# Kernel tuning notes

Hardware: AMD Instinct MI355X
Metric: run time of the kernel (lower is better)

Reference implementation:

```python
import jax, jax.numpy as jnp
from jax import lax
import numpy as np

# dims
B, S, IN, E = 2, 2048, 512, 1024
INNER = 2 * E              # mLSTM up-projection, proj_factor = 2.0
NH = 4                     # mLSTM cell heads
DH = INNER // NH           # 512
QKV_BLK = 4                # qkv_proj_blocksize
NHW = INNER // QKV_BLK     # heads of block-diagonal (headwise) q/k/v projections
K = 4                      # causal conv1d kernel size
EPS = 1e-6                 # mLSTM cell eps
LN_EPS = 1e-5


def setup_inputs() -> dict:
    key = jax.random.key(0)
    ks = jax.random.split(key, 16)
    n = lambda k, shp, s=0.02: jax.random.normal(k, shp, jnp.float32) * s
    z = lambda shp: jnp.zeros(shp, jnp.float32)
    return dict(
        x=jax.random.normal(ks[0], (B, S, IN), jnp.float32),
        w_in=n(ks[1], (IN, E)), b_in=z((E,)),
        ln1_w=jnp.ones((E,), jnp.float32),
        w_up=n(ks[2], (E, 2 * INNER)), b_up=z((2 * INNER,)),
        conv_w=n(ks[3], (INNER, K), 0.1), conv_b=z((INNER,)),
        q_w=n(ks[4], (NHW, QKV_BLK, QKV_BLK), 0.3), q_b=z((INNER,)),
        k_w=n(ks[5], (NHW, QKV_BLK, QKV_BLK), 0.3), k_b=z((INNER,)),
        v_w=n(ks[6], (NHW, QKV_BLK, QKV_BLK), 0.3), v_b=z((INNER,)),
        ig_w=n(ks[7], (3 * INNER, NH)), ig_b=z((NH,)),
        fg_w=n(ks[8], (3 * INNER, NH)), fg_b=jnp.ones((NH,), jnp.float32),
        onorm_w=jnp.ones((INNER,), jnp.float32),
        skip=n(ks[9], (INNER,), 1.0),
        w_down=n(ks[10], (INNER, E)), b_down=z((E,)),
        post_w=jnp.ones((E,), jnp.float32),
    )


def _layernorm(x, w, eps=LN_EPS):
    m = x.mean(-1, keepdims=True)
    v = x.var(-1, keepdims=True)
    return (x - m) / jnp.sqrt(v + eps) * w


def _headwise(x, w, b):
    # block-diagonal linear: x (B,S,INNER) split into NHW blocks of QKV_BLK
    Bx, Sx, _ = x.shape
    y = jnp.einsum('bshd,hod->bsho', x.reshape(Bx, Sx, NHW, QKV_BLK), w)
    return y.reshape(Bx, Sx, INNER) + b


def _mlstm_parallel(q, k, v, ig, fg):
    # q,k,v: (B,NH,S,DH); ig,fg: (B,NH,S). Parallel (stabilized) mLSTM.
    log_f = jax.nn.log_sigmoid(fg)                       # (B,NH,S)
    cum = jnp.cumsum(log_f, axis=-1)                     # inclusive cumsum
    dmat = cum[..., :, None] - cum[..., None, :]         # F_i - F_j  (B,NH,S,S)
    mask = jnp.tril(jnp.ones((S, S), bool))
    logD = jnp.where(mask, dmat + ig[..., None, :], -jnp.inf)
    m = logD.max(-1, keepdims=True)                      # (B,NH,S,1)
    Dm = jnp.exp(logD - m)
    qk = jnp.einsum('bnid,bnjd->bnij', q, k) / jnp.sqrt(jnp.float32(DH))
    C = qk * Dm
    norm = jnp.maximum(jnp.abs(C.sum(-1, keepdims=True)), jnp.exp(-m))
    return jnp.einsum('bnij,bnjd->bnid', C / (norm + EPS), v)


def _forward(x, w_in, b_in, ln1_w, w_up, b_up, conv_w, conv_b,
             q_w, q_b, k_w, k_b, v_w, v_b, ig_w, ig_b, fg_w, fg_b,
             onorm_w, skip, w_down, b_down, post_w):
    h_in = x @ w_in + b_in                               # (B,S,E); dropout = identity (eval)

    # --- mLSTM block: residual + pre-LN ---
    xn = _layernorm(h_in, ln1_w)
    up = xn @ w_up + b_up                                # (B,S,2*INNER)
    x_m, z = jnp.split(up, 2, axis=-1)

    # causal depthwise conv1d + SiLU
    rhs = conv_w.T[:, None, :]                           # (K,1,INNER)
    xc = lax.conv_general_dilated(x_m, rhs, window_strides=(1,),
                                  padding=[(K - 1, 0)],
                                  dimension_numbers=('NHC', 'HIO', 'NHC'),
                                  feature_group_count=INNER) + conv_b
    x_conv_act = jax.nn.silu(xc)

    q = _headwise(x_conv_act, q_w, q_b)                  # (B,S,INNER)
    k = _headwise(x_conv_act, k_w, k_b)
    v = _headwise(x_m, v_w, v_b)

    if_in = jnp.concatenate([q, k, v], axis=-1)          # (B,S,3*INNER)
    ig = (if_in @ ig_w + ig_b).transpose(0, 2, 1)        # (B,NH,S)
    fg = (if_in @ fg_w + fg_b).transpose(0, 2, 1)

    to_heads = lambda t: t.reshape(B, S, NH, DH).transpose(0, 2, 1, 3)
    h = _mlstm_parallel(to_heads(q), to_heads(k), to_heads(v), ig, fg)  # (B,NH,S,DH)

    # multi-head (group) norm over DH, then learned scale over flat features
    hn = (h - h.mean(-1, keepdims=True)) / jnp.sqrt(h.var(-1, keepdims=True) + LN_EPS)
    hn = hn.transpose(0, 2, 1, 3).reshape(B, S, INNER) * onorm_w

    h_skip = hn + skip * x_conv_act                      # learnable skip
    h_gated = h_skip * jax.nn.silu(z)                    # output gate
    y = h_gated @ w_down + b_down                        # (B,S,E)

    out = h_in + y                                       # residual
    return _layernorm(out, post_w)                       # post_blocks_norm


def reference(x, w_in, b_in, ln1_w, w_up, b_up, conv_w, conv_b,
              q_w, q_b, k_w, k_b, v_w, v_b, ig_w, ig_b, fg_w, fg_b,
              onorm_w, skip, w_down, b_down, post_w):
    return _forward(x, w_in, b_in, ln1_w, w_up, b_up, conv_w, conv_b,
                    q_w, q_b, k_w, k_b, v_w, v_b, ig_w, ig_b, fg_w, fg_b,
                    onorm_w, skip, w_down, b_down, post_w)
```

## Files before the change

### kernel.cpp

```cpp
#include <hip/hip_runtime.h>
#include <hip/hip_bf16.h>

typedef __hip_bfloat16 bf16;
typedef float floatx4 __attribute__((ext_vector_type(4)));
typedef short bf16x8 __attribute__((ext_vector_type(8)));

#define B_      2
#define S_      2048
#define IN_     512
#define E_      1024
#define INNER_  2048
#define NH_     4
#define DH_     512
#define T_      (B_*S_)
#define EPS_CELL 1e-6f
#define LN_EPS_  1e-5f
#define LS      72
#define CTB_    4

__device__ inline float b2f(bf16 x){ return __bfloat162float(x); }
__device__ inline bf16  f2b(float x){ return __float2bfloat16(x); }
__device__ inline float us2f(unsigned short u){ union{unsigned int i; float f;} v; v.i = ((unsigned int)u)<<16; return v.f; }
__device__ inline float u2f(unsigned int u){ union{unsigned int i; float f;} v; v.i = u; return v.f; }
__device__ inline unsigned short f2bu(float x){ bf16 t = __float2bfloat16(x); unsigned short r; __builtin_memcpy(&r,&t,2); return r; }
__device__ inline void unpack8(uint4 u, float* f){
  f[0]=u2f(u.x<<16); f[1]=u2f(u.x&0xffff0000u);
  f[2]=u2f(u.y<<16); f[3]=u2f(u.y&0xffff0000u);
  f[4]=u2f(u.z<<16); f[5]=u2f(u.z&0xffff0000u);
  f[6]=u2f(u.w<<16); f[7]=u2f(u.w&0xffff0000u);
}
__device__ inline uint4 pack8(const float* f){
  uint4 u;
  u.x = (unsigned)f2bu(f[0]) | ((unsigned)f2bu(f[1])<<16);
  u.y = (unsigned)f2bu(f[2]) | ((unsigned)f2bu(f[3])<<16);
  u.z = (unsigned)f2bu(f[4]) | ((unsigned)f2bu(f[5])<<16);
  u.w = (unsigned)f2bu(f[6]) | ((unsigned)f2bu(f[7])<<16);
  return u;
}
__device__ inline void stv(bf16* p, float v){ *p = f2b(v); }
__device__ inline void stv(float* p, float v){ *p = v; }

typedef __attribute__((address_space(3))) unsigned int lds_u32_t;
typedef __attribute__((address_space(1))) const unsigned int glb_u32_t;
__device__ __forceinline__ void cp_async16(const bf16* g, short* l){
  __builtin_amdgcn_global_load_lds((glb_u32_t*)(const void*)g,
                                   (lds_u32_t*)(void*)l, 16, 0, 0);
}
__device__ __forceinline__ int so_(int row, int c8){ return row*64 + (((c8) ^ (row&7))<<3); }
__device__ __forceinline__ int eo_(int row, int ch){ return row*128 + (((ch) ^ (row&15))<<3); }

#define STAGE_ASYNC(dst, srcbase, stride, kk) \
  { int slot_ = (kk)*256 + tid; int r_ = slot_>>3; int c8_ = (slot_&7) ^ (r_&7); \
    cp_async16((srcbase) + (size_t)r_*(stride) + c8_*8, &dst[slot_*8]); }

__global__ __launch_bounds__(256) void convert_bf16(const float* __restrict__ X,
    bf16* __restrict__ Y, int n8){
  int i = blockIdx.x*256 + threadIdx.x;
  if (i >= n8) return;
  const float4* p = (const float4*)(X) + i*2;
  float4 a = p[0], b = p[1];
  ushort4 o0, o1;
  o0.x=f2bu(a.x); o0.y=f2bu(a.y); o0.z=f2bu(a.z); o0.w=f2bu(a.w);
  o1.x=f2bu(b.x); o1.y=f2bu(b.y); o1.z=f2bu(b.z); o1.w=f2bu(b.w);
  ushort4* q = (ushort4*)(Y) + i*2;
  q[0]=o0; q[1]=o1;
}

__global__ __launch_bounds__(256) void transpose_conv_w(const float* __restrict__ W,
    bf16* __restrict__ Wt, int K, int N){
  int n0 = blockIdx.x*64, k0 = blockIdx.y*64;
  __shared__ float tl[64][65];
  int tid = threadIdx.x;
  #pragma unroll
  for (int i=0;i<4;i++){
    int idx = tid + i*256; int r = idx>>4, c4 = idx&15;
    float4 v = *(const float4*)(W + (size_t)(k0+r)*N + n0 + c4*4);
    tl[r][c4*4+0]=v.x; tl[r][c4*4+1]=v.y; tl[r][c4*4+2]=v.z; tl[r][c4*4+3]=v.w;
  }
  __syncthreads();
  #pragma unroll
  for (int i=0;i<4;i++){
    int idx = tid + i*256; int rn = idx>>4, c4 = idx&15;
    ushort4 o;
    o.x=f2bu(tl[c4*4+0][rn]); o.y=f2bu(tl[c4*4+1][rn]);
    o.z=f2bu(tl[c4*4+2][rn]); o.w=f2bu(tl[c4*4+3][rn]);
    *(ushort4*)(Wt + (size_t)(n0+rn)*K + k0 + c4*4) = o;
  }
}

__global__ __launch_bounds__(256) void mfma_gemm(const bf16* __restrict__ A,
    const bf16* __restrict__ Bt, const float* __restrict__ bias, bf16* __restrict__ C,
    int Kd, int lda, int ldc, int NN){
  int bid = blockIdx.x;
  int MM = gridDim.x / NN;
  int mPerX = MM >> 3;
  int xcd = bid & 7, seq = bid >> 3;
  int nb = seq % NN, mb = xcd*mPerX + seq / NN;
  int n0 = nb*128, m0 = mb*128;
  __shared__ __align__(16) short smem[32768];
  int tid = threadIdx.x;
  int w = tid>>6, l = tid&63, lq = l>>4, lr = l&15;
  int wm = (w>>1)*64, wn = (w&1)*64;
  const bf16* Abase = A + (size_t)m0*lda;
  const bf16* Bbase = Bt + (size_t)n0*Kd;
  floatx4 acc[4][4];
  #pragma unroll
  for (int mi=0;mi<4;mi++){
    #pragma unroll
    for (int ni=0;ni<4;ni++) acc[mi][ni] = (floatx4){0.f,0.f,0.f,0.f};
  }
  short* As0 = smem;          short* Bs0 = smem + 8192;
  short* As1 = smem + 16384;  short* Bs1 = smem + 24576;
  int NT = Kd >> 6;
  #pragma unroll
  for (int kk=0;kk<4;kk++){
    STAGE_ASYNC(As0, Abase, lda, kk);
    STAGE_ASYNC(Bs0, Bbase, Kd, kk);
  }
  __syncthreads();
  for (int t=0; t<NT; ++t){
    short* As  = (t&1) ? As1 : As0;
    short* Bs  = (t&1) ? Bs1 : Bs0;
    short* Asn = (t&1) ? As0 : As1;
    short* Bsn = (t&1) ? Bs0 : Bs1;
    if (t+1 < NT){
      int k0 = (t+1)*64;
      #pragma unroll
      for (int kk=0;kk<4;kk++){
        STAGE_ASYNC(Asn, Abase + k0, lda, kk);
        STAGE_ASYNC(Bsn, Bbase + k0, Kd, kk);
      }
    }
    #pragma unroll
    for (int ks=0; ks<2; ks++){
      bf16x8 af[4], bfr[4];
      #pragma unroll
      for (int mi=0;mi<4;mi++) af[mi] = *(const bf16x8*)&As[so_(wm+mi*16+lr, ks*4+lq)];
      #pragma unroll
      for (int ni=0;ni<4;ni++) bfr[ni] = *(const bf16x8*)&Bs[so_(wn+ni*16+lr, ks*4+lq)];
      #pragma unroll
      for (int mi=0;mi<4;mi++){
        #pragma unroll
        for (int ni=0;ni<4;ni++)
          acc[mi][ni] = __builtin_amdgcn_mfma_f32_16x16x32_bf16(af[mi], bfr[ni], acc[mi][ni], 0,0,0);
      }
    }
    __syncthreads();
  }
  float bb[4];
  #pragma unroll
  for (int ni=0;ni<4;ni++) bb[ni] = bias[n0 + wn + ni*16 + lr];
  #pragma unroll
  for (int mi=0;mi<4;mi++){
    #pragma unroll
    for (int ni=0;ni<4;ni++){
      int coll = wn + ni*16 + lr;
      int ch = coll>>3, off = coll&7;
      #pragma unroll
      for (int r=0;r<4;r++){
        int rowl = wm + mi*16 + lq*4 + r;
        smem[rowl*128 + (((ch) ^ (rowl&15))<<3) + off] = (short)f2bu(acc[mi][ni][r] + bb[ni]);
      }
    }
  }
  __syncthreads();
  #pragma unroll
  for (int i=0;i<8;i++){
    int slot = i*256 + tid;
    int r = slot >> 4, c8 = slot & 15;
    uint4 val = *(const uint4*)&smem[eo_(r, c8)];
    *(uint4*)(C + (size_t)(m0+r)*ldc + n0 + c8*8) = val;
  }
}

template<typename OutT>
__global__ __launch_bounds__(256) void ln_rows(const bf16* __restrict__ X,
    const bf16* __restrict__ Xadd, const float* __restrict__ w, OutT* __restrict__ Y){
  int row = blockIdx.x, tid = threadIdx.x;
  size_t base = (size_t)row*E_;
  float vals[4], s=0.f, s2=0.f;
  #pragma unroll
  for (int e=0;e<4;e++){
    int c = e*256+tid;
    float v = b2f(X[base+c]);
    if (Xadd) v += b2f(Xadd[base+c]);
    vals[e]=v; s+=v; s2+=v*v;
  }
  __shared__ float sa[256], sb[256];
  sa[tid]=s; sb[tid]=s2; __syncthreads();
  for (int off=128; off>0; off>>=1){
    if (tid<off){ sa[tid]+=sa[tid+off]; sb[tid]+=sb[tid+off]; }
    __syncthreads();
  }
  float mean = sa[0]*(1.f/E_);
  float var  = sb[0]*(1.f/E_) - mean*mean;
  float rstd = rsqrtf(var + LN_EPS_);
  #pragma unroll
  for (int e=0;e<4;e++){
    int c = e*256+tid;
    stv(&Y[base+c], (vals[e]-mean)*rstd*w[c]);
  }
}

__global__ __launch_bounds__(256) void conv_headwise(const bf16* __restrict__ up,
    const float* __restrict__ cw, const float* __restrict__ cb,
    const float* __restrict__ qw, const float* __restrict__ qb,
    const float* __restrict__ kw, const float* __restrict__ kb,
    const float* __restrict__ vw, const float* __restrict__ vb,
    bf16* __restrict__ xca, bf16* __restrict__ q, bf16* __restrict__ k,
    bf16* __restrict__ v){
  int t0 = blockIdx.x*CTB_;
  int s0 = t0 & (S_-1);
  int c0 = threadIdx.x*8;
  int hw0 = c0 >> 2;

  float row[7][8];
  #pragma unroll
  for (int j=0;j<7;j++){
    if (s0-3+j >= 0){
      uint4 rv = *(const uint4*)(up + (size_t)(t0-3+j)*(2*INNER_) + c0);
      unpack8(rv, row[j]);
    } else {
      #pragma unroll
      for (int e=0;e<8;e++) row[j][e]=0.f;
    }
  }

  float xc[CTB_][8];
  {
    float cwv[8][4], cbv[8];
    #pragma unroll
    for (int e=0;e<8;e++){
      float4 w4 = *(const float4*)(cw + (size_t)(c0+e)*4);
      cwv[e][0]=w4.x; cwv[e][1]=w4.y; cwv[e][2]=w4.z; cwv[e][3]=w4.w;
    }
    float4 b0 = *(const float4*)(cb+c0), b1 = *(const float4*)(cb+c0+4);
    cbv[0]=b0.x; cbv[1]=b0.y; cbv[2]=b0.z; cbv[3]=b0.w;
    cbv[4]=b1.x; cbv[5]=b1.y; cbv[6]=b1.z; cbv[7]=b1.w;
    #pragma unroll
    for (int i=0;i<CTB_;i++){
      #pragma unroll
      for (int e=0;e<8;e++){
        float a = cbv[e];
        #pragma unroll
        for (int t=0;t<4;t++) a += row[i+t][e]*cwv[e][t];
        xc[i][e] = a/(1.f+expf(-a));
      }
      *(uint4*)(xca + (size_t)(t0+i)*INNER_ + c0) = pack8(xc[i]);
    }
  }

  {
    float wv_[32], bv[8];
    #pragma unroll
    for (int g=0;g<2;g++){
      #pragma unroll
      for (int r4=0;r4<4;r4++){
        float4 w4 = *(const float4*)(vw + (size_t)(hw0+g)*16 + r4*4);
        wv_[g*16+r4*4+0]=w4.x; wv_[g*16+r4*4+1]=w4.y;
        wv_[g*16+r4*4+2]=w4.z; wv_[g*16+r4*4+3]=w4.w;
      }
    }
    float4 b0 = *(const float4*)(vb+c0), b1 = *(const float4*)(vb+c0+4);
    bv[0]=b0.x; bv[1]=b0.y; bv[2]=b0.z; bv[3]=b0.w;
    bv[4]=b1.x; bv[5]=b1.y; bv[6]=b1.z; bv[7]=b1.w;
    #pragma unroll
    for (int i=0;i<CTB_;i++){
      float ov[8];
      #pragma unroll
      for (int g=0;g<2;g++){
        #pragma unroll
        for (int o=0;o<4;o++){
          float a = bv[g*4+o];
          #pragma unroll
          for (int d=0;d<4;d++) a += row[i+3][g*4+d]*wv_[g*16+o*4+d];
          ov[g*4+o]=a;
        }
      }
      *(uint4*)(v + (size_t)(t0+i)*INNER_ + c0) = pack8(ov);
    }
  }

  {
    float wv_[32], bv[8];
    #pragma unroll
    for (int g=0;g<2;g++){
      #pragma unroll
      for (int r4=0;r4<4;r4++){
        float4 w4 = *(const float4*)(qw + (size_t)(hw0+g)*16 + r4*4);
        wv_[g*16+r4*4+0]=w4.x; wv_[g*16+r4*4+1]=w4.y;
        wv_[g*16+r4*4+2]=w4.z; wv_[g*16+r4*4+3]=w4.w;
      }
    }
    float4 b0 = *(const float4*)(qb+c0), b1 = *(const float4*)(qb+c0+4);
    bv[0]=b0.x; bv[1]=b0.y; bv[2]=b0.z; bv[3]=b0.w;
    bv[4]=b1.x; bv[5]=b1.y; bv[6]=b1.z; bv[7]=b1.w;
    #pragma unroll
    for (int i=0;i<CTB_;i++){
      float ov[8];
      #pragma unroll
      for (int g=0;g<2;g++){
        #pragma unroll
        for (int o=0;o<4;o++){
          float a = bv[g*4+o];
          #pragma unroll
          for (int d=0;d<4;d++) a += xc[i][g*4+d]*wv_[g*16+o*4+d];
          ov[g*4+o]=a;
        }
      }
      *(uint4*)(q + (size_t)(t0+i)*INNER_ + c0) = pack8(ov);
    }
  }

  {
    float wv_[32], bv[8];
    #pragma unroll
    for (int g=0;g<2;g++){
      #pragma unroll
      for (int r4=0;r4<4;r4++){
        float4 w4 = *(const float4*)(kw + (size_t)(hw0+g)*16 + r4*4);
        wv_[g*16+r4*4+0]=w4.x; wv_[g*16+r4*4+1]=w4.y;
        wv_[g*16+r4*4+2]=w4.z; wv_[g*16+r4*4+3]=w4.w;
      }
    }
    float4 b0 = *(const float4*)(kb+c0), b1 = *(const float4*)(kb+c0+4);
    bv[0]=b0.x; bv[1]=b0.y; bv[2]=b0.z; bv[3]=b0.w;
    bv[4]=b1.x; bv[5]=b1.y; bv[6]=b1.z; bv[7]=b1.w;
    #pragma unroll
    for (int i=0;i<CTB_;i++){
      float ov[8];
      #pragma unroll
      for (int g=0;g<2;g++){
        #pragma unroll
        for (int o=0;o<4;o++){
          float a = bv[g*4+o];
          #pragma unroll
          for (int d=0;d<4;d++) a += xc[i][g*4+d]*wv_[g*16+o*4+d];
          ov[g*4+o]=a;
        }
      }
      *(uint4*)(k + (size_t)(t0+i)*INNER_ + c0) = pack8(ov);
    }
  }
}

__global__ __launch_bounds__(256) void pack_gates_w(const float* __restrict__ igw,
    const float* __restrict__ fgw, bf16* __restrict__ gwb){
  int idx = blockIdx.x*256 + threadIdx.x;
  if (idx >= 3*INNER_) return;
  int g = idx >> 9;
  int e = (idx >> 6) & 7;
  int l = idx & 63;
  int r = g*512 + l*8 + e;
  float4 a = *(const float4*)(igw + (size_t)r*4);
  float4 b = *(const float4*)(fgw + (size_t)r*4);
  ushort4 o0, o1;
  o0.x=f2bu(a.x); o0.y=f2bu(a.y); o0.z=f2bu(a.z); o0.w=f2bu(a.w);
  o1.x=f2bu(b.x); o1.y=f2bu(b.y); o1.z=f2bu(b.z); o1.w=f2bu(b.w);
  *(ushort4*)(gwb + (size_t)idx*8)     = o0;
  *(ushort4*)(gwb + (size_t)idx*8 + 4) = o1;
}

__global__ __launch_bounds__(256) void gates_kernel(const bf16* __restrict__ q,
    const bf16* __restrict__ k, const bf16* __restrict__ v,
    const bf16* __restrict__ gwb, const float* __restrict__ igb,
    const float* __restrict__ fgb, float* __restrict__ igo, float* __restrict__ fgo){
  __shared__ float red[4*32];
  int tid = threadIdx.x;
  int w = tid >> 6, l = tid & 63;
  int quad = w >> 1, kh = w & 1;
  int tok0 = blockIdx.x*8 + quad*4;
  float acc[4][8];
  #pragma unroll
  for (int t=0;t<4;t++){
    #pragma unroll
    for (int n=0;n<8;n++) acc[t][n]=0.f;
  }
  #pragma unroll 2
  for (int it=0; it<6; ++it){
    int src = it >> 1, j = it & 1;
    const bf16* sp = (src==0) ? q : ((src==1) ? k : v);
    int pos = kh*1024 + j*512 + l*8;
    int g = src*4 + kh*2 + j;
    uint4 dv[4];
    #pragma unroll
    for (int t=0;t<4;t++)
      dv[t] = *(const uint4*)(sp + (size_t)(tok0+t)*INNER_ + pos);
    float d[4][8];
    #pragma unroll
    for (int t=0;t<4;t++) unpack8(dv[t], d[t]);
    const bf16* wb = gwb + (size_t)g*512*8;
    #pragma unroll
    for (int e=0;e<8;e++){
      uint4 wv = *(const uint4*)(wb + (size_t)(e*64 + l)*8);
      float w8[8]; unpack8(wv, w8);
      #pragma unroll
      for (int t=0;t<4;t++){
        #pragma unroll
        for (int n=0;n<8;n++) acc[t][n] += d[t][e]*w8[n];
      }
    }
  }
  #pragma unroll
  for (int off=1; off<64; off<<=1){
    #pragma unroll
    for (int t=0;t<4;t++){
      #pragma unroll
      for (int n=0;n<8;n++) acc[t][n] += __shfl_xor(acc[t][n], off);
    }
  }
  if (l == 0){
    #pragma unroll
    for (int t=0;t<4;t++){
      #pragma unroll
      for (int n=0;n<8;n++) red[w*32 + t*8 + n] = acc[t][n];
    }
  }
  __syncthreads();
  if (tid < 64){
    int qd = tid >> 5, tn = tid & 31;
    int t = tn >> 3, n = tn & 7;
    float val = red[(qd*2)*32 + tn] + red[(qd*2+1)*32 + tn];
    int tok = blockIdx.x*8 + qd*4 + t;
    int b = tok >> 11, s = tok & (S_-1);
    if (n < 4) igo[((size_t)(b*NH_+n))*S_ + s] = val + igb[n];
    else       fgo[((size_t)(b*NH_+(n-4)))*S_ + s] = val + fgb[n-4];
  }
}

__global__ __launch_bounds__(256) void scan8(const float* __restrict__ igp,
    const float* __restrict__ fgp, float* __restrict__ ap,
    float* __restrict__ Mp, float* __restrict__ flp, float* __restrict__ rowsum){
  int h = blockIdx.x, tid = threadIdx.x;
  const float* fg = fgp + (size_t)h*S_;
  const float* ig = igp + (size_t)h*S_;
  int base = tid*8;
  float loc[8], run = 0.f;
  #pragma unroll
  for (int e=0;e<8;e++){
    float x = fg[base+e];
    float ls = fminf(x,0.f) - log1pf(expf(-fabsf(x)));
    run += ls; loc[e] = run;
  }
  __shared__ float sd[256];
  sd[tid]=run; __syncthreads();
  if (tid==0){ float r=0.f; for(int t=0;t<256;t++){ float t0=sd[t]; sd[t]=r; r+=t0; } }
  __syncthreads();
  float off = sd[tid];
  float lm[8], rm = -3e38f;
  #pragma unroll
  for (int e=0;e<8;e++){
    float F = loc[e]+off; loc[e]=F;
    float aj = ig[base+e]-F;
    ap[(size_t)h*S_+base+e]=aj;
    rm = fmaxf(rm, aj); lm[e]=rm;
  }
  __syncthreads();
  sd[tid]=rm; __syncthreads();
  if (tid==0){ float r=-3e38f; for(int t=0;t<256;t++){ float t0=sd[t]; sd[t]=r; r=fmaxf(r,t0); } }
  __syncthreads();
  float offm = sd[tid];
  #pragma unroll
  for (int e=0;e<8;e++){
    float M = fmaxf(lm[e], offm);
    Mp[(size_t)h*S_+base+e]=M;
    flp[(size_t)h*S_+base+e]=expf(-loc[e]-M);
    rowsum[(size_t)h*S_+base+e]=0.f;
  }
}

__global__ __launch_bounds__(256) void transpose_v(const bf16* __restrict__ v,
    bf16* __restrict__ vT){
  int sb = blockIdx.x, db = blockIdx.y, h = blockIdx.z;
  int b = h >> 2, n = h & 3;
  int s0 = sb*64, d0 = db*64;
  __shared__ short tl[64*LS];
  int tid = threadIdx.x;
  #pragma unroll
  for (int i=0;i<2;i++){
    int vv = tid + i*256; int r = vv>>3, c8 = vv&7;
    uint4 x = *(const uint4*)(v + (size_t)(b*S_+s0+r)*INNER_ + n*DH_ + d0 + c8*8);
    *(uint4*)&tl[r*LS + c8*8] = x;
  }
  __syncthreads();
  #pragma unroll
  for (int i=0;i<2;i++){
    int vv = tid + i*256; int r = vv>>3, c8 = vv&7;
    unsigned short tmp[8];
    #pragma unroll
    for (int e=0;e<8;e++) tmp[e] = (unsigned short)tl[(c8*8+e)*LS + r];
    uint4 o; __builtin_memcpy(&o, tmp, 16);
    *(uint4*)(vT + ((size_t)h*DH_ + d0 + r)*S_ + s0 + c8*8) = o;
  }
}

__global__ __launch_bounds__(256) void qk_decay_kernel(const bf16* __restrict__ qg,
    const bf16* __restrict__ kg, const float* __restrict__ ap,
    const float* __restrict__ Mp, float* __restrict__ rowsum, bf16* __restrict__ W){
  int h = blockIdx.x & 7;
  int t = 271 - (blockIdx.x >> 3);
  int p = (int)((sqrtf(4.f*t+1.f)-1.f)*0.5f);
  while ((p+1)*(p+2) <= t) p++;
  while (p*(p+1) > t) p--;
  int r0 = t - p*(p+1);
  int nj = p + 1;
  int it = 2*p + (r0 >= nj ? 1 : 0);
  int tj = r0 >= nj ? r0 - nj : r0;
  int b = h >> 2, n = h & 3;
  int i0 = it*64, j0 = tj*128;
  __shared__ __align__(16) short smem[2*12288];
  __shared__ float a_s[128], m_s[64];
  int tid = threadIdx.x;
  if (tid < 128) a_s[tid] = ap[(size_t)h*S_ + j0 + tid];
  if (tid < 64)  m_s[tid] = Mp[(size_t)h*S_ + i0 + tid];
  int w = tid>>6, l = tid&63, lq = l>>4, lr = l&15;
  int wm = (w>>1)*32, wn = (w&1)*64;
  const bf16* Qbase = qg + (size_t)(b*S_+i0)*INNER_ + n*DH_;
  const bf16* Kbase = kg + (size_t)(b*S_+j0)*INNER_ + n*DH_;
  floatx4 acc[2][4];
  #pragma unroll
  for (int mi=0;mi<2;mi++){
    #pragma unroll
    for (int ni=0;ni<4;ni++) acc[mi][ni] = (floatx4){0.f,0.f,0.f,0.f};
  }
  short* Qs0 = smem;          short* Ks0 = smem + 4096;
  short* Qs1 = smem + 12288;  short* Ks1 = smem + 16384;
  STAGE_ASYNC(Qs0, Qbase, INNER_, 0);
  STAGE_ASYNC(Qs0, Qbase, INNER_, 1);
  #pragma unroll
  for (int kk=0;kk<4;kk++){ STAGE_ASYNC(Ks0, Kbase, INNER_, kk); }
  __syncthreads();
  const int NT = DH_/64;
  for (int tt=0; tt<NT; ++tt){
    short* Qs  = (tt&1) ? Qs1 : Qs0;
    short* Ks  = (tt&1) ? Ks1 : Ks0;
    short* Qsn = (tt&1) ? Qs0 : Qs1;
    short* Ksn = (tt&1) ? Ks0 : Ks1;
    if (tt+1 < NT){
      int d0 = (tt+1)*64;
      STAGE_ASYNC(Qsn, Qbase + d0, INNER_, 0);
      STAGE_ASYNC(Qsn, Qbase + d0, INNER_, 1);
      #pragma unroll
      for (int kk=0;kk<4;kk++){ STAGE_ASYNC(Ksn, Kbase + d0, INNER_, kk); }
    }
    #pragma unroll
    for (int ks=0; ks<2; ks++){
      bf16x8 af[2], bfr[4];
      #pragma unroll
      for (int mi=0;mi<2;mi++) af[mi] = *(const bf16x8*)&Qs[so_(wm+mi*16+lr, ks*4+lq)];
      #pragma unroll
      for (int ni=0;ni<4;ni++) bfr[ni] = *(const bf16x8*)&Ks[so_(wn+ni*16+lr, ks*4+lq)];
      #pragma unroll
      for (int mi=0;mi<2;mi++){
        #pragma unroll
        for (int ni=0;ni<4;ni++)
          acc[mi][ni] = __builtin_amdgcn_mfma_f32_16x16x32_bf16(af[mi], bfr[ni], acc[mi][ni], 0,0,0);
      }
    }
    __syncthreads();
  }
  const float scale = 0.04419417382415922f;
  float rpart[2][4];
  #pragma unroll
  for (int mi=0;mi<2;mi++){
    #pragma unroll
    for (int r=0;r<4;r++) rpart[mi][r]=0.f;
  }
  #pragma unroll
  for (int mi=0;mi<2;mi++){
    #pragma unroll
    for (int ni=0;ni<4;ni++){
      int coll = wn + ni*16 + lr;
      int ch = coll>>3, off = coll&7;
      float av = a_s[coll];
      #pragma unroll
      for (int r=0;r<4;r++){
        int rowl = wm + mi*16 + lq*4 + r;
        int gi = i0 + rowl, gj = j0 + coll;
        float wv = 0.f;
        if (gj <= gi) wv = acc[mi][ni][r]*scale*__expf(av-m_s[rowl]);
        smem[rowl*128 + (((ch) ^ (rowl&15))<<3) + off] = (short)f2bu(wv);
        rpart[mi][r] += wv;
      }
    }
  }
  __syncthreads();
  #pragma unroll
  for (int i=0;i<4;i++){
    int slot = i*256 + tid;
    int r = slot >> 4, c8 = slot & 15;
    uint4 val = *(const uint4*)&smem[eo_(r, c8)];
    *(uint4*)(W + ((size_t)h*S_ + i0 + r)*S_ + j0 + c8*8) = val;
  }
  #pragma unroll
  for (int mi=0;mi<2;mi++){
    #pragma unroll
    for (int r=0;r<4;r++){
      float v = rpart[mi][r];
      v += __shfl_xor(v, 1, 16);
      v += __shfl_xor(v, 2, 16);
      v += __shfl_xor(v, 4, 16);
      v += __shfl_xor(v, 8, 16);
      if (lr == 0)
        atomicAdd(&rowsum[(size_t)h*S_ + i0 + wm + mi*16 + lq*4 + r], v);
    }
  }
}

__global__ __launch_bounds__(256) void pv_kernel(const bf16* __restrict__ W,
    const bf16* __restrict__ vT, const float* __restrict__ rowsum,
    const float* __restrict__ fl, bf16* __restrict__ O){
  int h = blockIdx.x & 7;
  int s = blockIdx.x >> 3;
  int ti = 31 - (s >> 2), tn = s & 3;
  int b = h >> 2, n = h & 3;
  int i0 = ti*64, d0 = tn*128;
  __shared__ __align__(16) short smem[2*12288];
  __shared__ float inv_s[64];
  int tid = threadIdx.x;
  if (tid < 64){
    size_t o = (size_t)h*S_ + i0 + tid;
    inv_s[tid] = 1.f/(fmaxf(fabsf(rowsum[o]), fl[o]) + EPS_CELL);
  }
  int w = tid>>6, l = tid&63, lq = l>>4, lr = l&15;
  int wm = (w>>1)*32, wn = (w&1)*64;
  const bf16* Wbase = W + ((size_t)h*S_ + i0)*S_;
  const bf16* Vbase = vT + ((size_t)h*DH_ + d0)*S_;
  floatx4 acc[2][4];
  #pragma unroll
  for (int mi=0;mi<2;mi++){
    #pragma unroll
    for (int ni=0;ni<4;ni++) acc[mi][ni] = (floatx4){0.f,0.f,0.f,0.f};
  }
  short* Ws0 = smem;          short* Vs0 = smem + 4096;
  short* Ws1 = smem + 12288;  short* Vs1 = smem + 16384;
  int NT = (i0 >> 6) + 1;
  STAGE_ASYNC(Ws0, Wbase, S_, 0);
  STAGE_ASYNC(Ws0, Wbase, S_, 1);
  #pragma unroll
  for (int kk=0;kk<4;kk++){ STAGE_ASYNC(Vs0, Vbase, S_, kk); }
  __syncthreads();
  for (int tt=0; tt<NT; ++tt){
    short* Ws  = (tt&1) ? Ws1 : Ws0;
    short* Vs  = (tt&1) ? Vs1 : Vs0;
    short* Wsn = (tt&1) ? Ws0 : Ws1;
    short* Vsn = (tt&1) ? Vs0 : Vs1;
    if (tt+1 < NT){
      int j0 = (tt+1)*64;
      STAGE_ASYNC(Wsn, Wbase + j0, S_, 0);
      STAGE_ASYNC(Wsn, Wbase + j0, S_, 1);
      #pragma unroll
      for (int kk=0;kk<4;kk++){ STAGE_ASYNC(Vsn, Vbase + j0, S_, kk); }
    }
    #pragma unroll
    for (int ks=0; ks<2; ks++){
      bf16x8 af[2], bfr[4];
      #pragma unroll
      for (int mi=0;mi<2;mi++) af[mi] = *(const bf16x8*)&Ws[so_(wm+mi*16+lr, ks*4+lq)];
      #pragma unroll
      for (int ni=0;ni<4;ni++) bfr[ni] = *(const bf16x8*)&Vs[so_(wn+ni*16+lr, ks*4+lq)];
      #pragma unroll
      for (int mi=0;mi<2;mi++){
        #pragma unroll
        for (int ni=0;ni<4;ni++)
          acc[mi][ni] = __builtin_amdgcn_mfma_f32_16x16x32_bf16(af[mi], bfr[ni], acc[mi][ni], 0,0,0);
      }
    }
    __syncthreads();
  }
  #pragma unroll
  for (int mi=0;mi<2;mi++){
    #pragma unroll
    for (int ni=0;ni<4;ni++){
      int dl = wn + ni*16 + lr;
      int ch = dl>>3, off = dl&7;
      #pragma unroll
      for (int r=0;r<4;r++){
        int rowl = wm + mi*16 + lq*4 + r;
        smem[rowl*128 + (((ch) ^ (rowl&15))<<3) + off] = (short)f2bu(acc[mi][ni][r] * inv_s[rowl]);
      }
    }
  }
  __syncthreads();
  #pragma unroll
  for (int i=0;i<4;i++){
    int slot = i*256 + tid;
    int r = slot >> 4, c8 = slot & 15;
    uint4 val = *(const uint4*)&smem[eo_(r, c8)];
    *(uint4*)(O + (size_t)(b*S_ + i0 + r)*INNER_ + n*DH_ + d0 + c8*8) = val;
  }
}

__global__ __launch_bounds__(256) void headnorm_gate(const bf16* __restrict__ h,
    const float* __restrict__ onw, const float* __restrict__ skip,
    const bf16* __restrict__ xca, bf16* __restrict__ up){
  int bid = blockIdx.x;
  int n = bid & 3; int bs = bid >> 2;
  int tid = threadIdx.x;
  size_t hbase = (size_t)bs*INNER_ + n*DH_;
  float v0 = b2f(h[hbase+tid]);
  float v1 = b2f(h[hbase+256+tid]);
  __shared__ float sa[256], sb[256];
  sa[tid]=v0+v1; sb[tid]=v0*v0+v1*v1;
  __syncthreads();
  for (int off=128; off>0; off>>=1){
    if (tid<off){ sa[tid]+=sa[tid+off]; sb[tid]+=sb[tid+off]; }
    __syncthreads();
  }
  float mean = sa[0]*(1.f/DH_);
  float var  = sb[0]*(1.f/DH_) - mean*mean;
  float rstd = rsqrtf(var + LN_EPS_);
  #pragma unroll
  for (int e=0;e<2;e++){
    int dl = e*256+tid; int c = n*DH_+dl;
    float hv = e ? v1 : v0;
    float hn = (hv-mean)*rstd*onw[c];
    float hs = hn + skip[c]*b2f(xca[(size_t)bs*INNER_+c]);
    size_t zoff = (size_t)bs*(2*INNER_) + INNER_ + c;
    float zv = b2f(up[zoff]);
    float sz = zv/(1.f+expf(-zv));
    up[zoff] = f2b(hs*sz);
  }
}

extern "C" void kernel_launch(void* const* d_in, const int* in_sizes, int n_in,
                              void* d_out, int out_size, void* d_ws, size_t ws_size,
                              hipStream_t stream) {
  const float* x      = (const float*)d_in[0];
  const float* w_in   = (const float*)d_in[1];
  const float* b_in   = (const float*)d_in[2];
  const float* ln1_w  = (const float*)d_in[3];
  const float* w_up   = (const float*)d_in[4];
  const float* b_up   = (const float*)d_in[5];
  const float* conv_w = (const float*)d_in[6];
  const float* conv_b = (const float*)d_in[7];
  const float* q_w    = (const float*)d_in[8];
  const float* q_b    = (const float*)d_in[9];
  const float* k_w    = (const float*)d_in[10];
  const float* k_b    = (const float*)d_in[11];
  const float* v_w    = (const float*)d_in[12];
  const float* v_b    = (const float*)d_in[13];
  const float* ig_w   = (const float*)d_in[14];
  const float* ig_b   = (const float*)d_in[15];
  const float* fg_w   = (const float*)d_in[16];
  const float* fg_b   = (const float*)d_in[17];
  const float* onw    = (const float*)d_in[18];
  const float* skip   = (const float*)d_in[19];
  const float* w_down = (const float*)d_in[20];
  const float* b_down = (const float*)d_in[21];
  const float* post_w = (const float*)d_in[22];

  char* p = (char*)d_ws;
  auto alloc = [&](size_t bytes)->void*{ void* r = p; p += (bytes + 255) & ~(size_t)255; return r; };
  bf16* h_in = (bf16*)alloc((size_t)T_*E_*2);
  bf16* xn   = (bf16*)alloc((size_t)T_*E_*2);
  bf16* up   = (bf16*)alloc((size_t)T_*2*INNER_*2);
  bf16* xca  = (bf16*)alloc((size_t)T_*INNER_*2);
  bf16* qb_  = (bf16*)alloc((size_t)T_*INNER_*2);
  bf16* kb_  = (bf16*)alloc((size_t)T_*INNER_*2);
  bf16* vb_  = (bf16*)alloc((size_t)T_*INNER_*2);
  bf16* hb_  = (bf16*)alloc((size_t)T_*INNER_*2);
  float* igbuf = (float*)alloc((size_t)B_*NH_*S_*4);
  float* fgbuf = (float*)alloc((size_t)B_*NH_*S_*4);
  float* abuf  = (float*)alloc((size_t)B_*NH_*S_*4);
  float* Mbuf  = (float*)alloc((size_t)B_*NH_*S_*4);
  float* flbuf = (float*)alloc((size_t)B_*NH_*S_*4);
  float* rsbuf = (float*)alloc((size_t)B_*NH_*S_*4);
  bf16* gwb  = (bf16*)alloc((size_t)3*INNER_*8*2);
  bf16* Wbuf = (bf16*)alloc((size_t)B_*NH_*S_*S_*2);
  bf16* ybuf = xn;
  bf16* vTb  = hb_;
  bf16* obuf = vb_;
  bf16* xbf    = Wbuf;
  bf16* w_in_t = Wbuf + (size_t)T_*IN_;
  bf16* w_up_t = w_in_t + (size_t)E_*IN_;
  bf16* w_down_t = Wbuf;

  convert_bf16<<<(T_*IN_/8+255)/256, 256, 0, stream>>>(x, xbf, T_*IN_/8);
  transpose_conv_w<<<dim3(E_/64, IN_/64), 256, 0, stream>>>(w_in, w_in_t, IN_, E_);
  transpose_conv_w<<<dim3((2*INNER_)/64, E_/64), 256, 0, stream>>>(w_up, w_up_t, E_, 2*INNER_);
  pack_gates_w<<<(3*INNER_+255)/256, 256, 0, stream>>>(ig_w, fg_w, gwb);
  mfma_gemm<<<(T_/128)*(E_/128), 256, 0, stream>>>(xbf, w_in_t, b_in, h_in, IN_, IN_, E_, E_/128);
  ln_rows<bf16><<<T_, 256, 0, stream>>>(h_in, nullptr, ln1_w, xn);
  mfma_gemm<<<(T_/128)*((2*INNER_)/128), 256, 0, stream>>>(xn, w_up_t, b_up, up, E_, E_, 2*INNER_, (2*INNER_)/128);
  conv_headwise<<<T_/CTB_, 256, 0, stream>>>(up, conv_w, conv_b,
      q_w, q_b, k_w, k_b, v_w, v_b, xca, qb_, kb_, vb_);
  gates_kernel<<<T_/8, 256, 0, stream>>>(qb_, kb_, vb_, gwb, ig_b, fg_b, igbuf, fgbuf);
  scan8<<<B_*NH_, 256, 0, stream>>>(igbuf, fgbuf, abuf, Mbuf, flbuf, rsbuf);
  transpose_v<<<dim3(S_/64, DH_/64, B_*NH_), 256, 0, stream>>>(vb_, vTb);
  qk_decay_kernel<<<8*272, 256, 0, stream>>>(qb_, kb_, abuf, Mbuf, rsbuf, Wbuf);
  pv_kernel<<<8*128, 256, 0, stream>>>(Wbuf, vTb, rsbuf, flbuf, obuf);
  headnorm_gate<<<T_*NH_, 256, 0, stream>>>(obuf, onw, skip, xca, up);
  transpose_conv_w<<<dim3(E_/64, INNER_/64), 256, 0, stream>>>(w_down, w_down_t, INNER_, E_);
  mfma_gemm<<<(T_/128)*(E_/128), 256, 0, stream>>>(up + INNER_, w_down_t, b_down, ybuf, INNER_, 2*INNER_, E_, E_/128);
  ln_rows<float><<<T_, 256, 0, stream>>>(h_in, ybuf, post_w, (float*)d_out);
}
```

Before: 377.5 us.

## Merge prep and transpose kernels by block range; use 64-row GEMM tiles for small GEMMs

Several small independent kernels are merged into combined launches that pick their work by block index. The x/weight conversion, weight transposes and gate-weight packing become one kernel. The gates reduction is fused with the V transpose, and the head-norm is fused with the w_down transpose. The two N=1024 GEMMs switch to a 64-row M tile, doubling the block count (256 to 512) to fill more CUs, at the cost of less reuse per tile. The goal is fewer launches and less tail idle time, with some added divergence inside the merged kernels.

```diff
diff --git a/kernel.cpp b/kernel.cpp
--- a/kernel.cpp
+++ b/kernel.cpp
@@ -20,7 +20,6 @@
 
 __device__ inline float b2f(bf16 x){ return __bfloat162float(x); }
 __device__ inline bf16  f2b(float x){ return __float2bfloat16(x); }
-__device__ inline float us2f(unsigned short u){ union{unsigned int i; float f;} v; v.i = ((unsigned int)u)<<16; return v.f; }
 __device__ inline float u2f(unsigned int u){ union{unsigned int i; float f;} v; v.i = u; return v.f; }
 __device__ inline unsigned short f2bu(float x){ bf16 t = __float2bfloat16(x); unsigned short r; __builtin_memcpy(&r,&t,2); return r; }
 __device__ inline void unpack8(uint4 u, float* f){
@@ -53,24 +52,8 @@
   { int slot_ = (kk)*256 + tid; int r_ = slot_>>3; int c8_ = (slot_&7) ^ (r_&7); \
     cp_async16((srcbase) + (size_t)r_*(stride) + c8_*8, &dst[slot_*8]); }
 
-__global__ __launch_bounds__(256) void convert_bf16(const float* __restrict__ X,
-    bf16* __restrict__ Y, int n8){
-  int i = blockIdx.x*256 + threadIdx.x;
-  if (i >= n8) return;
-  const float4* p = (const float4*)(X) + i*2;
-  float4 a = p[0], b = p[1];
-  ushort4 o0, o1;
-  o0.x=f2bu(a.x); o0.y=f2bu(a.y); o0.z=f2bu(a.z); o0.w=f2bu(a.w);
-  o1.x=f2bu(b.x); o1.y=f2bu(b.y); o1.z=f2bu(b.z); o1.w=f2bu(b.w);
-  ushort4* q = (ushort4*)(Y) + i*2;
-  q[0]=o0; q[1]=o1;
-}
-
-__global__ __launch_bounds__(256) void transpose_conv_w(const float* __restrict__ W,
-    bf16* __restrict__ Wt, int K, int N){
-  int n0 = blockIdx.x*64, k0 = blockIdx.y*64;
-  __shared__ float tl[64][65];
-  int tid = threadIdx.x;
+__device__ inline void transpose_tile(const float* W, bf16* Wt, int K, int N,
+    int n0, int k0, int tid, float (*tl)[65]){
   #pragma unroll
   for (int i=0;i<4;i++){
     int idx = tid + i*256; int r = idx>>4, c4 = idx&15;
@@ -85,6 +68,48 @@
     o.x=f2bu(tl[c4*4+0][rn]); o.y=f2bu(tl[c4*4+1][rn]);
     o.z=f2bu(tl[c4*4+2][rn]); o.w=f2bu(tl[c4*4+3][rn]);
     *(ushort4*)(Wt + (size_t)(n0+rn)*K + k0 + c4*4) = o;
+  }
+}
+
+__global__ __launch_bounds__(256) void prep_fused(const float* __restrict__ x,
+    const float* __restrict__ w_in, const float* __restrict__ w_up,
+    const float* __restrict__ igw, const float* __restrict__ fgw,
+    bf16* __restrict__ xbf, bf16* __restrict__ w_in_t, bf16* __restrict__ w_up_t,
+    bf16* __restrict__ gwb){
+  __shared__ float tl[64][65];
+  int bid = blockIdx.x, tid = threadIdx.x;
+  if (bid < 1024){
+    int i = bid*256 + tid;
+    const float4* p = (const float4*)(x) + i*2;
+    float4 a = p[0], b = p[1];
+    ushort4 o0, o1;
+    o0.x=f2bu(a.x); o0.y=f2bu(a.y); o0.z=f2bu(a.z); o0.w=f2bu(a.w);
+    o1.x=f2bu(b.x); o1.y=f2bu(b.y); o1.z=f2bu(b.z); o1.w=f2bu(b.w);
+    ushort4* q = (ushort4*)(xbf) + i*2;
+    q[0]=o0; q[1]=o1;
+  } else if (bid < 1152){
+    int id = bid - 1024;
+    int n0 = (id & 15)*64, k0 = (id >> 4)*64;
+    transpose_tile(w_in, w_in_t, IN_, E_, n0, k0, tid, tl);
+  } else if (bid < 2176){
+    int id = bid - 1152;
+    int n0 = (id & 63)*64, k0 = (id >> 6)*64;
+    transpose_tile(w_up, w_up_t, E_, 2*INNER_, n0, k0, tid, tl);
+  } else {
+    int idx = (bid - 2176)*256 + tid;
+    if (idx < 3*INNER_){
+      int g = idx >> 9;
+      int e = (idx >> 6) & 7;
+      int l = idx & 63;
+      int r = g*512 + l*8 + e;
+      float4 a = *(const float4*)(igw + (size_t)r*4);
+      float4 b = *(const float4*)(fgw + (size_t)r*4);
+      ushort4 o0, o1;
+      o0.x=f2bu(a.x); o0.y=f2bu(a.y); o0.z=f2bu(a.z); o0.w=f2bu(a.w);
+      o1.x=f2bu(b.x); o1.y=f2bu(b.y); o1.z=f2bu(b.z); o1.w=f2bu(b.w);
+      *(ushort4*)(gwb + (size_t)idx*8)     = o0;
+      *(ushort4*)(gwb + (size_t)idx*8 + 4) = o1;
+    }
   }
 }
 
@@ -173,6 +198,89 @@
   }
 }
 
+__global__ __launch_bounds__(256) void mfma_gemm64(const bf16* __restrict__ A,
+    const bf16* __restrict__ Bt, const float* __restrict__ bias, bf16* __restrict__ C,
+    int Kd, int lda, int ldc, int NN){
+  int bid = blockIdx.x;
+  int MM = gridDim.x / NN;
+  int mPerX = MM >> 3;
+  int xcd = bid & 7, seq = bid >> 3;
+  int nb = seq % NN, mb = xcd*mPerX + seq / NN;
+  int n0 = nb*128, m0 = mb*64;
+  __shared__ __align__(16) short smem[24576];
+  int tid = threadIdx.x;
+  int w = tid>>6, l = tid&63, lq = l>>4, lr = l&15;
+  int wm = (w>>1)*32, wn = (w&1)*64;
+  const bf16* Abase = A + (size_t)m0*lda;
+  const bf16* Bbase = Bt + (size_t)n0*Kd;
+  floatx4 acc[2][4];
+  #pragma unroll
+  for (int mi=0;mi<2;mi++){
+    #pragma unroll
+    for (int ni=0;ni<4;ni++) acc[mi][ni] = (floatx4){0.f,0.f,0.f,0.f};
+  }
+  short* As0 = smem;          short* Bs0 = smem + 4096;
+  short* As1 = smem + 12288;  short* Bs1 = smem + 16384;
+  int NT = Kd >> 6;
+  STAGE_ASYNC(As0, Abase, lda, 0);
+  STAGE_ASYNC(As0, Abase, lda, 1);
+  #pragma unroll
+  for (int kk=0;kk<4;kk++){ STAGE_ASYNC(Bs0, Bbase, Kd, kk); }
+  __syncthreads();
+  for (int t=0; t<NT; ++t){
+    short* As  = (t&1) ? As1 : As0;
+    short* Bs  = (t&1) ? Bs1 : Bs0;
+    short* Asn = (t&1) ? As0 : As1;
+    short* Bsn = (t&1) ? Bs0 : Bs1;
+    if (t+1 < NT){
+      int k0 = (t+1)*64;
+      STAGE_ASYNC(Asn, Abase + k0, lda, 0);
+      STAGE_ASYNC(Asn, Abase + k0, lda, 1);
+      #pragma unroll
+      for (int kk=0;kk<4;kk++){ STAGE_ASYNC(Bsn, Bbase + k0, Kd, kk); }
+    }
+    #pragma unroll
+    for (int ks=0; ks<2; ks++){
+      bf16x8 af[2], bfr[4];
+      #pragma unroll
+      for (int mi=0;mi<2;mi++) af[mi] = *(const bf16x8*)&As[so_(wm+mi*16+lr, ks*4+lq)];
+      #pragma unroll
+      for (int ni=0;ni<4;ni++) bfr[ni] = *(const bf16x8*)&Bs[so_(wn+ni*16+lr, ks*4+lq)];
+      #pragma unroll
+      for (int mi=0;mi<2;mi++){
+        #pragma unroll
+        for (int ni=0;ni<4;ni++)
+          acc[mi][ni] = __builtin_amdgcn_mfma_f32_16x16x32_bf16(af[mi], bfr[ni], acc[mi][ni], 0,0,0);
+      }
+    }
+    __syncthreads();
+  }
+  float bb[4];
+  #pragma unroll
+  for (int ni=0;ni<4;ni++) bb[ni] = bias[n0 + wn + ni*16 + lr];
+  #pragma unroll
+  for (int mi=0;mi<2;mi++){
+    #pragma unroll
+    for (int ni=0;ni<4;ni++){
+      int coll = wn + ni*16 + lr;
+      int ch = coll>>3, off = coll&7;
+      #pragma unroll
+      for (int r=0;r<4;r++){
+        int rowl = wm + mi*16 + lq*4 + r;
+        smem[rowl*128 + (((ch) ^ (rowl&15))<<3) + off] = (short)f2bu(acc[mi][ni][r] + bb[ni]);
+      }
+    }
+  }
+  __syncthreads();
+  #pragma unroll
+  for (int i=0;i<4;i++){
+    int slot = i*256 + tid;
+    int r = slot >> 4, c8 = slot & 15;
+    uint4 val = *(const uint4*)&smem[eo_(r, c8)];
+    *(uint4*)(C + (size_t)(m0+r)*ldc + n0 + c8*8) = val;
+  }
+}
+
 template<typename OutT>
 __global__ __launch_bounds__(256) void ln_rows(const bf16* __restrict__ X,
     const bf16* __restrict__ Xadd, const float* __restrict__ w, OutT* __restrict__ Y){
@@ -344,87 +452,95 @@
   }
 }
 
-__global__ __launch_bounds__(256) void pack_gates_w(const float* __restrict__ igw,
-    const float* __restrict__ fgw, bf16* __restrict__ gwb){
-  int idx = blockIdx.x*256 + threadIdx.x;
-  if (idx >= 3*INNER_) return;
-  int g = idx >> 9;
-  int e = (idx >> 6) & 7;
-  int l = idx & 63;
-  int r = g*512 + l*8 + e;
-  float4 a = *(const float4*)(igw + (size_t)r*4);
-  float4 b = *(const float4*)(fgw + (size_t)r*4);
-  ushort4 o0, o1;
-  o0.x=f2bu(a.x); o0.y=f2bu(a.y); o0.z=f2bu(a.z); o0.w=f2bu(a.w);
-  o1.x=f2bu(b.x); o1.y=f2bu(b.y); o1.z=f2bu(b.z); o1.w=f2bu(b.w);
-  *(ushort4*)(gwb + (size_t)idx*8)     = o0;
-  *(ushort4*)(gwb + (size_t)idx*8 + 4) = o1;
-}
-
-__global__ __launch_bounds__(256) void gates_kernel(const bf16* __restrict__ q,
+__global__ __launch_bounds__(256) void gates_transv(const bf16* __restrict__ q,
     const bf16* __restrict__ k, const bf16* __restrict__ v,
     const bf16* __restrict__ gwb, const float* __restrict__ igb,
-    const float* __restrict__ fgb, float* __restrict__ igo, float* __restrict__ fgo){
+    const float* __restrict__ fgb, float* __restrict__ igo, float* __restrict__ fgo,
+    bf16* __restrict__ vT){
   __shared__ float red[4*32];
-  int tid = threadIdx.x;
-  int w = tid >> 6, l = tid & 63;
-  int quad = w >> 1, kh = w & 1;
-  int tok0 = blockIdx.x*8 + quad*4;
-  float acc[4][8];
-  #pragma unroll
-  for (int t=0;t<4;t++){
-    #pragma unroll
-    for (int n=0;n<8;n++) acc[t][n]=0.f;
-  }
-  #pragma unroll 2
-  for (int it=0; it<6; ++it){
-    int src = it >> 1, j = it & 1;
-    const bf16* sp = (src==0) ? q : ((src==1) ? k : v);
-    int pos = kh*1024 + j*512 + l*8;
-    int g = src*4 + kh*2 + j;
-    uint4 dv[4];
-    #pragma unroll
-    for (int t=0;t<4;t++)
-      dv[t] = *(const uint4*)(sp + (size_t)(tok0+t)*INNER_ + pos);
-    float d[4][8];
-    #pragma unroll
-    for (int t=0;t<4;t++) unpack8(dv[t], d[t]);
-    const bf16* wb = gwb + (size_t)g*512*8;
-    #pragma unroll
-    for (int e=0;e<8;e++){
-      uint4 wv = *(const uint4*)(wb + (size_t)(e*64 + l)*8);
-      float w8[8]; unpack8(wv, w8);
+  __shared__ short tl[64*LS];
+  int bid = blockIdx.x, tid = threadIdx.x;
+  if (bid < 512){
+    int w = tid >> 6, l = tid & 63;
+    int quad = w >> 1, kh = w & 1;
+    int tok0 = bid*8 + quad*4;
+    float acc[4][8];
+    #pragma unroll
+    for (int t=0;t<4;t++){
+      #pragma unroll
+      for (int n=0;n<8;n++) acc[t][n]=0.f;
+    }
+    #pragma unroll 2
+    for (int it=0; it<6; ++it){
+      int src = it >> 1, j = it & 1;
+      const bf16* sp = (src==0) ? q : ((src==1) ? k : v);
+      int pos = kh*1024 + j*512 + l*8;
+      int g = src*4 + kh*2 + j;
+      uint4 dv[4];
+      #pragma unroll
+      for (int t=0;t<4;t++)
+        dv[t] = *(const uint4*)(sp + (size_t)(tok0+t)*INNER_ + pos);
+      float d[4][8];
+      #pragma unroll
+      for (int t=0;t<4;t++) unpack8(dv[t], d[t]);
+      const bf16* wb = gwb + (size_t)g*512*8;
+      #pragma unroll
+      for (int e=0;e<8;e++){
+        uint4 wv = *(const uint4*)(wb + (size_t)(e*64 + l)*8);
+        float w8[8]; unpack8(wv, w8);
+        #pragma unroll
+        for (int t=0;t<4;t++){
+          #pragma unroll
+          for (int n=0;n<8;n++) acc[t][n] += d[t][e]*w8[n];
+        }
+      }
+    }
+    #pragma unroll
+    for (int off=1; off<64; off<<=1){
       #pragma unroll
       for (int t=0;t<4;t++){
         #pragma unroll
-        for (int n=0;n<8;n++) acc[t][n] += d[t][e]*w8[n];
-      }
-    }
-  }
-  #pragma unroll
-  for (int off=1; off<64; off<<=1){
-    #pragma unroll
-    for (int t=0;t<4;t++){
-      #pragma unroll
-      for (int n=0;n<8;n++) acc[t][n] += __shfl_xor(acc[t][n], off);
-    }
-  }
-  if (l == 0){
-    #pragma unroll
-    for (int t=0;t<4;t++){
-      #pragma unroll
-      for (int n=0;n<8;n++) red[w*32 + t*8 + n] = acc[t][n];
-    }
-  }
-  __syncthreads();
-  if (tid < 64){
-    int qd = tid >> 5, tn = tid & 31;
-    int t = tn >> 3, n = tn & 7;
-    float val = red[(qd*2)*32 + tn] + red[(qd*2+1)*32 + tn];
-    int tok = blockIdx.x*8 + qd*4 + t;
-    int b = tok >> 11, s = tok & (S_-1);
-    if (n < 4) igo[((size_t)(b*NH_+n))*S_ + s] = val + igb[n];
-    else       fgo[((size_t)(b*NH_+(n-4)))*S_ + s] = val + fgb[n-4];
+        for (int n=0;n<8;n++) acc[t][n] += __shfl_xor(acc[t][n], off);
+      }
+    }
+    if (l == 0){
+      #pragma unroll
+      for (int t=0;t<4;t++){
+        #pragma unroll
+        for (int n=0;n<8;n++) red[w*32 + t*8 + n] = acc[t][n];
+      }
+    }
+    __syncthreads();
+    if (tid < 64){
+      int qd = tid >> 5, tn = tid & 31;
+      int t = tn >> 3, n = tn & 7;
+      float val = red[(qd*2)*32 + tn] + red[(qd*2+1)*32 + tn];
+      int tok = bid*8 + qd*4 + t;
+      int b = tok >> 11, s = tok & (S_-1);
+      if (n < 4) igo[((size_t)(b*NH_+n))*S_ + s] = val + igb[n];
+      else       fgo[((size_t)(b*NH_+(n-4)))*S_ + s] = val + fgb[n-4];
+    }
+  } else {
+    int id = bid - 512;
+    int sb = id & 31, db = (id >> 5) & 7, h = id >> 8;
+    int b = h >> 2, n = h & 3;
+    int s0 = sb*64, d0 = db*64;
+    #pragma unroll
+    for (int i=0;i<2;i++){
+      int vv = tid + i*256; int r = vv>>3, c8 = vv&7;
+      uint4 x = *(const uint4*)(v + (size_t)(b*S_+s0+r)*INNER_ + n*DH_ + d0 + c8*8);
+      *(uint4*)&tl[r*LS + c8*8] = x;
+    }
+    __syncthreads();
+    #pragma unroll
+    for (int i=0;i<2;i++){
+      int vv = tid + i*256; int r = vv>>3, c8 = vv&7;
+      unsigned short tmp[8];
+      #pragma unroll
+      for (int e=0;e<8;e++) tmp[e] = (unsigned short)tl[(c8*8+e)*LS + r];
+      uint4 o; __builtin_memcpy(&o, tmp, 16);
+      *(uint4*)(vT + ((size_t)h*DH_ + d0 + r)*S_ + s0 + c8*8) = o;
+    }
   }
 }
 
@@ -466,31 +582,6 @@
     Mp[(size_t)h*S_+base+e]=M;
     flp[(size_t)h*S_+base+e]=expf(-loc[e]-M);
     rowsum[(size_t)h*S_+base+e]=0.f;
-  }
-}
-
-__global__ __launch_bounds__(256) void transpose_v(const bf16* __restrict__ v,
-    bf16* __restrict__ vT){
-  int sb = blockIdx.x, db = blockIdx.y, h = blockIdx.z;
-  int b = h >> 2, n = h & 3;
-  int s0 = sb*64, d0 = db*64;
-  __shared__ short tl[64*LS];
-  int tid = threadIdx.x;
-  #pragma unroll
-  for (int i=0;i<2;i++){
-    int vv = tid + i*256; int r = vv>>3, c8 = vv&7;
-    uint4 x = *(const uint4*)(v + (size_t)(b*S_+s0+r)*INNER_ + n*DH_ + d0 + c8*8);
-    *(uint4*)&tl[r*LS + c8*8] = x;
-  }
-  __syncthreads();
-  #pragma unroll
-  for (int i=0;i<2;i++){
-    int vv = tid + i*256; int r = vv>>3, c8 = vv&7;
-    unsigned short tmp[8];
-    #pragma unroll
-    for (int e=0;e<8;e++) tmp[e] = (unsigned short)tl[(c8*8+e)*LS + r];
-    uint4 o; __builtin_memcpy(&o, tmp, 16);
-    *(uint4*)(vT + ((size_t)h*DH_ + d0 + r)*S_ + s0 + c8*8) = o;
   }
 }
 
@@ -691,16 +782,23 @@
   }
 }
 
-__global__ __launch_bounds__(256) void headnorm_gate(const bf16* __restrict__ h,
+__global__ __launch_bounds__(256) void headnorm_wdown(const bf16* __restrict__ h,
     const float* __restrict__ onw, const float* __restrict__ skip,
-    const bf16* __restrict__ xca, bf16* __restrict__ up){
-  int bid = blockIdx.x;
-  int n = bid & 3; int bs = bid >> 2;
-  int tid = threadIdx.x;
+    const bf16* __restrict__ xca, bf16* __restrict__ up,
+    const float* __restrict__ w_down, bf16* __restrict__ w_down_t){
+  __shared__ float sa[256], sb[256];
+  __shared__ float tl[64][65];
+  int bid = blockIdx.x, tid = threadIdx.x;
+  if (bid < 512){
+    int n0 = (bid & 15)*64, k0 = (bid >> 4)*64;
+    transpose_tile(w_down, w_down_t, INNER_, E_, n0, k0, tid, tl);
+    return;
+  }
+  int id = bid - 512;
+  int n = id & 3; int bs = id >> 2;
   size_t hbase = (size_t)bs*INNER_ + n*DH_;
   float v0 = b2f(h[hbase+tid]);
   float v1 = b2f(h[hbase+256+tid]);
-  __shared__ float sa[256], sb[256];
   sa[tid]=v0+v1; sb[tid]=v0*v0+v1*v1;
   __syncthreads();
   for (int off=128; off>0; off>>=1){
@@ -776,22 +874,20 @@
   bf16* w_up_t = w_in_t + (size_t)E_*IN_;
   bf16* w_down_t = Wbuf;
 
-  convert_bf16<<<(T_*IN_/8+255)/256, 256, 0, stream>>>(x, xbf, T_*IN_/8);
-  transpose_conv_w<<<dim3(E_/64, IN_/64), 256, 0, stream>>>(w_in, w_in_t, IN_, E_);
-  transpose_conv_w<<<dim3((2*INNER_)/64, E_/64), 256, 0, stream>>>(w_up, w_up_t, E_, 2*INNER_);
-  pack_gates_w<<<(3*INNER_+255)/256, 256, 0, stream>>>(ig_w, fg_w, gwb);
-  mfma_gemm<<<(T_/128)*(E_/128), 256, 0, stream>>>(xbf, w_in_t, b_in, h_in, IN_, IN_, E_, E_/128);
+  prep_fused<<<2200, 256, 0, stream>>>(x, w_in, w_up, ig_w, fg_w,
+      xbf, w_in_t, w_up_t, gwb);
+  mfma_gemm64<<<(T_/64)*(E_/128), 256, 0, stream>>>(xbf, w_in_t, b_in, h_in, IN_, IN_, E_, E_/128);
   ln_rows<bf16><<<T_, 256, 0, stream>>>(h_in, nullptr, ln1_w, xn);
   mfma_gemm<<<(T_/128)*((2*INNER_)/128), 256, 0, stream>>>(xn, w_up_t, b_up, up, E_, E_, 2*INNER_, (2*INNER_)/128);
   conv_headwise<<<T_/CTB_, 256, 0, stream>>>(up, conv_w, conv_b,
       q_w, q_b, k_w, k_b, v_w, v_b, xca, qb_, kb_, vb_);
-  gates_kernel<<<T_/8, 256, 0, stream>>>(qb_, kb_, vb_, gwb, ig_b, fg_b, igbuf, fgbuf);
+  gates_transv<<<512 + 2048, 256, 0, stream>>>(qb_, kb_, vb_, gwb, ig_b, fg_b,
+      igbuf, fgbuf, vTb);
   scan8<<<B_*NH_, 256, 0, stream>>>(igbuf, fgbuf, abuf, Mbuf, flbuf, rsbuf);
-  transpose_v<<<dim3(S_/64, DH_/64, B_*NH_), 256, 0, stream>>>(vb_, vTb);
   qk_decay_kernel<<<8*272, 256, 0, stream>>>(qb_, kb_, abuf, Mbuf, rsbuf, Wbuf);
   pv_kernel<<<8*128, 256, 0, stream>>>(Wbuf, vTb, rsbuf, flbuf, obuf);
-  headnorm_gate<<<T_*NH_, 256, 0, stream>>>(obuf, onw, skip, xca, up);
-  transpose_conv_w<<<dim3(E_/64, INNER_/64), 256, 0, stream>>>(w_down, w_down_t, INNER_, E_);
-  mfma_gemm<<<(T_/128)*(E_/128), 256, 0, stream>>>(up + INNER_, w_down_t, b_down, ybuf, INNER_, 2*INNER_, E_, E_/128);
+  headnorm_wdown<<<512 + T_*NH_, 256, 0, stream>>>(obuf, onw, skip, xca, up,
+      w_down, w_down_t);
+  mfma_gemm64<<<(T_/64)*(E_/128), 256, 0, stream>>>(up + INNER_, w_down_t, b_down, ybuf, INNER_, 2*INNER_, E_, E_/128);
   ln_rows<float><<<T_, 256, 0, stream>>>(h_in, ybuf, post_w, (float*)d_out);
 }
```

Result: no change. 373.3 us (-1.1%).
